# Kernel tuning notes

Measured on AMD Instinct MI355X. Metric: run time of the kernel, lower is better.

Reference implementation:

```python
import jax, jax.numpy as jnp
import numpy as np

HEADS = 8

def setup_inputs() -> dict:
    key = jax.random.key(0)
    ks = jax.random.split(key, 11)
    B, S, E = 4, 2048, 512
    sc = 1.0 / np.sqrt(E)
    return {
        "inputs": jax.random.normal(ks[0], (B, S, E), jnp.float32),
        "entangle": jax.random.uniform(ks[1], (S,), jnp.float32),
        "Wq": jax.random.normal(ks[2], (E, E), jnp.float32) * sc,
        "bq": jax.random.normal(ks[3], (E,), jnp.float32) * 0.01,
        "Wk": jax.random.normal(ks[4], (E, E), jnp.float32) * sc,
        "bk": jax.random.normal(ks[5], (E,), jnp.float32) * 0.01,
        "Wv": jax.random.normal(ks[6], (E, E), jnp.float32) * sc,
        "bv": jax.random.normal(ks[7], (E,), jnp.float32) * 0.01,
        "Wo": jax.random.normal(ks[8], (E, E), jnp.float32) * sc,
        "bo": jax.random.normal(ks[9], (E,), jnp.float32) * 0.01,
    }

def reference(inputs, entangle, Wq, bq, Wk, bk, Wv, bv, Wo, bo):
    B, S, E = inputs.shape
    H = HEADS
    D = E // H
    # torch nn.Linear: y = x @ W.T + b
    Q = (inputs @ Wq.T + bq).reshape(B, S, H, D)
    K = (inputs @ Wk.T + bk).reshape(B, S, H, D)
    V = (inputs @ Wv.T + bv).reshape(B, S, H, D)
    scores = jnp.einsum('bqhd,bkhd->bhqk', Q, K) / jnp.sqrt(jnp.float32(D))
    # entangle broadcast as (1,1,S,1): per-query-position scaling before softmax
    scores = scores * entangle[None, None, :, None]
    attn = jax.nn.softmax(scores, axis=-1)
    out = jnp.einsum('bhqk,bkhd->bqhd', attn, V).reshape(B, S, E)
    return out @ Wo.T + bo
```

## Files before the change

### kernel.cpp

```cpp
#include <hip/hip_runtime.h>
#include <hip/hip_bf16.h>

#define BB 4
#define SS 2048
#define EE 512
#define HH 8
#define DD 64

typedef __attribute__((ext_vector_type(8))) short bf16x8;
typedef __attribute__((ext_vector_type(4))) float f32x4;
typedef __attribute__((ext_vector_type(4))) unsigned int u32x4;

__device__ __forceinline__ unsigned short f2bf(float f) {
    __hip_bfloat16 h = __float2bfloat16(f);
    return *reinterpret_cast<unsigned short*>(&h);
}

__device__ __forceinline__ unsigned int cvtpk(float lo, float hi) {
    unsigned int r;
    asm("v_cvt_pk_bf16_f32 %0, %1, %2" : "=v"(r) : "v"(lo), "v"(hi));
    return r;
}

__device__ __forceinline__ float ex2(float x) {
    float r;
    asm("v_exp_f32 %0, %1" : "=v"(r) : "v"(x));
    return r;
}

__device__ __forceinline__ void pl32(unsigned int& a, unsigned int& b) {
    asm("v_permlane32_swap_b32 %0, %1" : "+v"(a), "+v"(b));
}
__device__ __forceinline__ void pl16(unsigned int& a, unsigned int& b) {
    asm("v_permlane16_swap_b32 %0, %1" : "+v"(a), "+v"(b));
}

__device__ __forceinline__ void gll16(const unsigned short* g, unsigned short* l) {
    __builtin_amdgcn_global_load_lds(
        (const __attribute__((address_space(1))) unsigned int*)g,
        (__attribute__((address_space(3))) unsigned int*)l,
        16, 0, 0);
}

__global__ __launch_bounds__(256)
void cast_all(const float* __restrict__ x,
              const float* __restrict__ wq, const float* __restrict__ wk,
              const float* __restrict__ wv, const float* __restrict__ wo,
              unsigned short* __restrict__ xb,
              unsigned short* __restrict__ wqb, unsigned short* __restrict__ wkb,
              unsigned short* __restrict__ wvb, unsigned short* __restrict__ wob)
{
    const int bid = blockIdx.x;
    const float* src; unsigned short* dst; int lb;
    if (bid < 4096)      { src = x;  dst = xb;  lb = bid; }
    else {
        const int t = (bid - 4096) >> 8;
        lb = (bid - 4096) & 255;
        switch (t) {
            case 0:  src = wq; dst = wqb; break;
            case 1:  src = wk; dst = wkb; break;
            case 2:  src = wv; dst = wvb; break;
            default: src = wo; dst = wob; break;
        }
    }
    const int i = lb * 256 + threadIdx.x;
    const float4 v = reinterpret_cast<const float4*>(src)[i];
    ushort4 o;
    o.x = f2bf(v.x); o.y = f2bf(v.y); o.z = f2bf(v.z); o.w = f2bf(v.w);
    reinterpret_cast<ushort4*>(dst)[i] = o;
}

template<typename OutT, bool TRANSPOSE_V, int TM>
__global__ __launch_bounds__(256)
void gemm_mfma_nt(const unsigned short* __restrict__ A,
                  const unsigned short* __restrict__ W0, const float* __restrict__ b0, OutT* __restrict__ C0,
                  const unsigned short* __restrict__ W1, const float* __restrict__ b1, OutT* __restrict__ C1,
                  const unsigned short* __restrict__ W2, const float* __restrict__ b2, OutT* __restrict__ C2,
                  const float* __restrict__ rowscale,
                  int M, int N, int K)
{
    const unsigned short* W = (blockIdx.z == 0) ? W0 : (blockIdx.z == 1) ? W1 : W2;
    const float* bias       = (blockIdx.z == 0) ? b0 : (blockIdx.z == 1) ? b1 : b2;
    OutT* C                 = (blockIdx.z == 0) ? C0 : (blockIdx.z == 1) ? C1 : C2;

    constexpr int MT  = TM / 32;
    constexpr int STG = 3 * TM * 32;
    __shared__ unsigned short lds[STG + 3 * 128 * 32];
    unsigned short* As = lds;
    unsigned short* Bs = lds + STG;

    const int tid  = threadIdx.x;
    const int wave = tid >> 6, lane = tid & 63;
    const int quad = lane >> 4, r16 = lane & 15;
    const int m0 = blockIdx.x * TM, n0 = blockIdx.y * 128;
    const int wm0 = (wave >> 1) * (TM / 2), wn0 = (wave & 1) * 64;

    f32x4 acc[MT][4];
    const f32x4 zero = {0.f, 0.f, 0.f, 0.f};
    #pragma unroll
    for (int i = 0; i < MT; ++i)
        #pragma unroll
        for (int j = 0; j < 4; ++j) acc[i][j] = zero;

    const int swz = (r16 >> 1) & 3;

    auto stage = [&](int bi, int k0) {
        #pragma unroll
        for (int j = 0; j < TM / 64; ++j) {
            const int cb = wave * 64 + j * 256;
            const int c  = cb + lane;
            const int row = c >> 2, cc = (c & 3) ^ ((row >> 1) & 3);
            gll16(&A[(size_t)(m0 + row) * K + k0 + cc * 8], &As[bi * TM * 32 + cb * 8]);
        }
        #pragma unroll
        for (int j = 0; j < 2; ++j) {
            const int cb = wave * 64 + j * 256;
            const int c  = cb + lane;
            const int row = c >> 2, cc = (c & 3) ^ ((row >> 1) & 3);
            gll16(&W[(size_t)(n0 + row) * K + k0 + cc * 8], &Bs[bi * 128 * 32 + cb * 8]);
        }
    };

    stage(0, 0);
    stage(1, 32);

    const int NI = K / 32;
    for (int i = 0; i < NI; ++i) {
        const int cur = i % 3;
        if (i + 1 < NI) {
            if constexpr (TM == 128) asm volatile("s_waitcnt vmcnt(4)" ::: "memory");
            else                     asm volatile("s_waitcnt vmcnt(3)" ::: "memory");
        } else {
            asm volatile("s_waitcnt vmcnt(0)" ::: "memory");
        }
        __builtin_amdgcn_s_barrier();
        __builtin_amdgcn_sched_barrier(0);
        if (i + 2 < NI) stage((i + 2) % 3, (i + 2) * 32);

        bf16x8 af[MT], bfr[4];
        #pragma unroll
        for (int t = 0; t < MT; ++t)
            af[t]  = *reinterpret_cast<bf16x8*>(&As[cur * TM * 32 + ((wm0 + t * 16 + r16) * 4 + (quad ^ swz)) * 8]);
        #pragma unroll
        for (int t = 0; t < 4; ++t)
            bfr[t] = *reinterpret_cast<bf16x8*>(&Bs[cur * 128 * 32 + ((wn0 + t * 16 + r16) * 4 + (quad ^ swz)) * 8]);
        #pragma unroll
        for (int mt = 0; mt < MT; ++mt)
            #pragma unroll
            for (int nt = 0; nt < 4; ++nt)
                acc[mt][nt] = __builtin_amdgcn_mfma_f32_16x16x32_bf16(
                    af[mt], bfr[nt], acc[mt][nt], 0, 0, 0);
    }

    if (TRANSPOSE_V && blockIdx.z == 2) {
        __syncthreads();
        #pragma unroll
        for (int mt = 0; mt < MT; ++mt) {
            const int s_local = wm0 + mt * 16 + quad * 4;
            #pragma unroll
            for (int nt = 0; nt < 4; ++nt) {
                const int d_local = wn0 + nt * 16 + r16;
                const float bv = bias[n0 + d_local];
                uint2 o;
                o.x = cvtpk(acc[mt][nt][0] + bv, acc[mt][nt][1] + bv);
                o.y = cvtpk(acc[mt][nt][2] + bv, acc[mt][nt][3] + bv);
                *reinterpret_cast<uint2*>(&lds[d_local * 132 + s_local]) = o;
            }
        }
        __syncthreads();
        const int bb = m0 >> 11, s0 = m0 & (SS - 1);
        unsigned short* Vtp = (unsigned short*)C2 + (size_t)bb * EE * SS + s0;
        const int scol = (tid & 15) * 8;
        #pragma unroll
        for (int p = 0; p < 8; ++p) {
            const int row = p * 16 + (tid >> 4);
            const uint2 lo = *reinterpret_cast<const uint2*>(&lds[row * 132 + scol]);
            const uint2 hi = *reinterpret_cast<const uint2*>(&lds[row * 132 + scol + 4]);
            const u32x4 v = {lo.x, lo.y, hi.x, hi.y};
            *reinterpret_cast<u32x4*>(&Vtp[(size_t)(n0 + row) * SS + scol]) = v;
        }
        return;
    }
    if constexpr (sizeof(OutT) == 2) {
        const bool doscale = (rowscale != nullptr) && (blockIdx.z == 0);
        __syncthreads();
        #pragma unroll
        for (int mt = 0; mt < MT; ++mt) {
            float rs[4];
            #pragma unroll
            for (int r = 0; r < 4; ++r) {
                const int row = m0 + wm0 + mt * 16 + quad * 4 + r;
                rs[r] = doscale ? rowscale[row & (SS - 1)] * 0.18033688f : 1.0f;
            }
            #pragma unroll
            for (int nt = 0; nt < 4; ++nt) {
                const int col = wn0 + nt * 16 + r16;
                const float bv = bias[n0 + col];
                #pragma unroll
                for (int r = 0; r < 4; ++r) {
                    const int row = wm0 + mt * 16 + quad * 4 + r;
                    lds[row * 132 + col] = f2bf((acc[mt][nt][r] + bv) * rs[r]);
                }
            }
        }
        __syncthreads();
        const int scol = (tid & 15) * 8;
        #pragma unroll
        for (int p = 0; p < TM / 16; ++p) {
            const int row = p * 16 + (tid >> 4);
            const uint2 lo = *reinterpret_cast<const uint2*>(&lds[row * 132 + scol]);
            const uint2 hi = *reinterpret_cast<const uint2*>(&lds[row * 132 + scol + 4]);
            const u32x4 v = {lo.x, lo.y, hi.x, hi.y};
            *reinterpret_cast<u32x4*>(&((unsigned short*)C)[(size_t)(m0 + row) * N + n0 + scol]) = v;
        }
    } else {
        const bool doscale = (rowscale != nullptr) && (blockIdx.z == 0);
        #pragma unroll
        for (int mt = 0; mt < MT; ++mt) {
            float rs[4];
            #pragma unroll
            for (int r = 0; r < 4; ++r) {
                const int row = m0 + wm0 + mt * 16 + quad * 4 + r;
                rs[r] = doscale ? rowscale[row & (SS - 1)] * 0.18033688f : 1.0f;
            }
            #pragma unroll
            for (int nt = 0; nt < 4; ++nt) {
                const int col = n0 + wn0 + nt * 16 + r16;
                const float bv = bias[col];
                #pragma unroll
                for (int r = 0; r < 4; ++r) {
                    const int row = m0 + wm0 + mt * 16 + quad * 4 + r;
                    C[(size_t)row * N + col] = (OutT)((acc[mt][nt][r] + bv) * rs[r]);
                }
            }
        }
    }
}

#define QBLK 128

__global__ __launch_bounds__(256)
void attn_mfma(const unsigned short* __restrict__ Q,
               const unsigned short* __restrict__ K,
               const unsigned short* __restrict__ Vt,
               unsigned short* __restrict__ O)
{
    __shared__ unsigned short Ks[3][72 * 64];
    __shared__ unsigned short Vs[3][72 * 64];

    const int tid  = threadIdx.x;
    const int wave = tid >> 6, lane = tid & 63;
    const int quad = lane >> 4, r16 = lane & 15;
    const int h  = blockIdx.x;
    const int q0 = blockIdx.y * QBLK;
    const int b  = blockIdx.z;
    const size_t base    = (size_t)b * SS * EE + (size_t)h * DD;
    const size_t base_vt = ((size_t)b * HH + h) * DD * SS;

    bf16x8 qf[2][2];
    #pragma unroll
    for (int s = 0; s < 2; ++s) {
        const int qrow = q0 + s * 64 + wave * 16 + r16;
        #pragma unroll
        for (int dh = 0; dh < 2; ++dh)
            qf[s][dh] = *reinterpret_cast<const bf16x8*>(
                &Q[base + (size_t)qrow * EE + dh * 32 + quad * 8]);
    }

    const int cb0 = wave * 64, cb1 = wave * 64 + 256;
    const int c0 = cb0 + lane, c1 = cb1 + lane;
    const int row0 = c0 >> 3, cc0 = (c0 & 7) ^ (row0 & 7);
    const int row1 = c1 >> 3, cc1 = (c1 & 7) ^ (row1 & 7);
    const unsigned short* kp0 = &K[base + (size_t)row0 * EE + cc0 * 8];
    const unsigned short* kp1 = &K[base + (size_t)row1 * EE + cc1 * 8];
    const unsigned short* vp0 = &Vt[base_vt + (size_t)row0 * SS + cc0 * 8];
    const unsigned short* vp1 = &Vt[base_vt + (size_t)row1 * SS + cc1 * 8];

    auto stage = [&](int bi, int kt) {
        const size_t ko = (size_t)kt * 64 * EE;
        const int    vo = kt * 64;
        gll16(kp0 + ko, &Ks[bi][cb0 * 8]);
        gll16(vp0 + vo, &Vs[bi][cb0 * 8]);
        gll16(kp1 + ko, &Ks[bi][cb1 * 8]);
        gll16(vp1 + vo, &Vs[bi][cb1 * 8]);
    };

    float l_lane[2] = {0.f, 0.f};
    f32x4 o_acc[2][4];
    const f32x4 zero = {0.f, 0.f, 0.f, 0.f};
    #pragma unroll
    for (int s = 0; s < 2; ++s)
        #pragma unroll
        for (int dt = 0; dt < 4; ++dt) o_acc[s][dt] = zero;

    const int swz = r16 & 7;

    stage(0, 0);
    stage(1, 1);

    constexpr int NT = SS / 64;
    for (int kt = 0; kt < NT; ++kt) {
        const int cur = kt % 3;
        if (kt + 1 < NT) asm volatile("s_waitcnt vmcnt(4)" ::: "memory");
        else             asm volatile("s_waitcnt vmcnt(0)" ::: "memory");
        __builtin_amdgcn_s_barrier();
        __builtin_amdgcn_sched_barrier(0);
        if (kt + 2 < NT) stage((kt + 2) % 3, kt + 2);

        const unsigned short* Kc = &Ks[cur][0];
        const unsigned short* Vc = &Vs[cur][0];

        bf16x8 kfA[4], kfB[4];
        #pragma unroll
        for (int tn = 0; tn < 4; ++tn) {
            kfA[tn] = *reinterpret_cast<const bf16x8*>(&Kc[((tn * 16 + r16) * 8 + (quad ^ swz)) * 8]);
            kfB[tn] = *reinterpret_cast<const bf16x8*>(&Kc[((tn * 16 + r16) * 8 + ((quad + 4) ^ swz)) * 8]);
        }

        f32x4 st[2][4];
        #pragma unroll
        for (int s = 0; s < 2; ++s)
            #pragma unroll
            for (int tn = 0; tn < 4; ++tn) st[s][tn] = zero;
        __builtin_amdgcn_s_setprio(1);
        #pragma unroll
        for (int s = 0; s < 2; ++s)
            #pragma unroll
            for (int tn = 0; tn < 4; ++tn) {
                st[s][tn] = __builtin_amdgcn_mfma_f32_16x16x32_bf16(kfA[tn], qf[s][0], st[s][tn], 0, 0, 0);
                st[s][tn] = __builtin_amdgcn_mfma_f32_16x16x32_bf16(kfB[tn], qf[s][1], st[s][tn], 0, 0, 0);
            }
        __builtin_amdgcn_s_setprio(0);

        bf16x8 vfA[4], vfB[4];
        #pragma unroll
        for (int dt = 0; dt < 4; ++dt) {
            vfA[dt] = *reinterpret_cast<const bf16x8*>(&Vc[((dt * 16 + r16) * 8 + (quad ^ swz)) * 8]);
            vfB[dt] = *reinterpret_cast<const bf16x8*>(&Vc[((dt * 16 + r16) * 8 + ((quad + 4) ^ swz)) * 8]);
        }

        #pragma unroll
        for (int s = 0; s < 2; ++s) {
            unsigned int w[4][2];
            #pragma unroll
            for (int tn = 0; tn < 4; ++tn) {
                const float p0 = ex2(st[s][tn][0]);
                const float p1 = ex2(st[s][tn][1]);
                const float p2 = ex2(st[s][tn][2]);
                const float p3 = ex2(st[s][tn][3]);
                l_lane[s] += (p0 + p1) + (p2 + p3);
                w[tn][0] = cvtpk(p0, p1);
                w[tn][1] = cvtpk(p2, p3);
            }
            unsigned int pa0 = w[0][0], pa2 = w[1][0];
            pl32(pa0, pa2); pl16(pa0, pa2);
            unsigned int pa1 = w[0][1], pa3 = w[1][1];
            pl32(pa1, pa3); pl16(pa1, pa3);
            unsigned int pb0 = w[2][0], pb2 = w[3][0];
            pl32(pb0, pb2); pl16(pb0, pb2);
            unsigned int pb1 = w[2][1], pb3 = w[3][1];
            pl32(pb1, pb3); pl16(pb1, pb3);

            const u32x4 ua = {pa0, pa1, pa2, pa3};
            const u32x4 ub = {pb0, pb1, pb2, pb3};
            const bf16x8 pf0 = __builtin_bit_cast(bf16x8, ua);
            const bf16x8 pf1 = __builtin_bit_cast(bf16x8, ub);

            __builtin_amdgcn_s_setprio(1);
            #pragma unroll
            for (int dt = 0; dt < 4; ++dt) {
                o_acc[s][dt] = __builtin_amdgcn_mfma_f32_16x16x32_bf16(pf0, vfA[dt], o_acc[s][dt], 0, 0, 0);
                o_acc[s][dt] = __builtin_amdgcn_mfma_f32_16x16x32_bf16(pf1, vfB[dt], o_acc[s][dt], 0, 0, 0);
            }
            __builtin_amdgcn_s_setprio(0);
        }
    }

    float lq[2];
    #pragma unroll
    for (int s = 0; s < 2; ++s) {
        float l = l_lane[s];
        l += __shfl_xor(l, 16, 64);
        l += __shfl_xor(l, 32, 64);
        lq[s] = l;
    }

    unsigned short* ob = &Ks[0][0];
    __syncthreads();
    #pragma unroll
    for (int s = 0; s < 2; ++s) {
        #pragma unroll
        for (int r = 0; r < 4; ++r) {
            const float il = 1.0f / __shfl(lq[s], quad * 4 + r, 64);
            const int ql = s * 64 + wave * 16 + quad * 4 + r;
            #pragma unroll
            for (int dt = 0; dt < 4; ++dt)
                ob[ql * 68 + dt * 16 + r16] = f2bf(o_acc[s][dt][r] * il);
        }
    }
    __syncthreads();
    const int orow = tid >> 3, ocol = (tid & 7) * 8;
    #pragma unroll
    for (int p = 0; p < 4; ++p) {
        const int ql = p * 32 + orow;
        const uint2 lo = *reinterpret_cast<const uint2*>(&ob[ql * 68 + ocol]);
        const uint2 hi = *reinterpret_cast<const uint2*>(&ob[ql * 68 + ocol + 4]);
        const u32x4 v = {lo.x, lo.y, hi.x, hi.y};
        *reinterpret_cast<u32x4*>(&O[base + (size_t)(q0 + ql) * EE + ocol]) = v;
    }
}

extern "C" void kernel_launch(void* const* d_in, const int* in_sizes, int n_in,
                              void* d_out, int out_size, void* d_ws, size_t ws_size,
                              hipStream_t stream) {
    const float* x   = (const float*)d_in[0];
    const float* ent = (const float*)d_in[1];
    const float* Wq  = (const float*)d_in[2];
    const float* bq  = (const float*)d_in[3];
    const float* Wk  = (const float*)d_in[4];
    const float* bk  = (const float*)d_in[5];
    const float* Wv  = (const float*)d_in[6];
    const float* bv  = (const float*)d_in[7];
    const float* Wo  = (const float*)d_in[8];
    const float* bo  = (const float*)d_in[9];
    float* out = (float*)d_out;

    const size_t n_x = (size_t)BB * SS * EE;
    const size_t n_w = (size_t)EE * EE;

    unsigned short* xb  = (unsigned short*)d_ws;
    unsigned short* wqb = xb + n_x;
    unsigned short* wkb = wqb + n_w;
    unsigned short* wvb = wkb + n_w;
    unsigned short* wob = wvb + n_w;
    unsigned short* Qb  = wob + n_w;
    unsigned short* Kb  = Qb + n_x;
    unsigned short* Vtb = Kb + n_x;
    unsigned short* AOb = Vtb + n_x;

    const int M = BB * SS;

    dim3 gc(4096 + 4 * 256, 1, 1);
    cast_all<<<gc, 256, 0, stream>>>(x, Wq, Wk, Wv, Wo, xb, wqb, wkb, wvb, wob);

    dim3 gq(M / 128, EE / 128, 3);
    gemm_mfma_nt<unsigned short, true, 128><<<gq, 256, 0, stream>>>(
        xb, wqb, bq, Qb, wkb, bk, Kb, wvb, bv, Vtb, ent, M, EE, EE);

    dim3 ga(HH, SS / QBLK, BB);
    attn_mfma<<<ga, 256, 0, stream>>>(Qb, Kb, Vtb, AOb);

    dim3 go(M / 64, EE / 128, 1);
    gemm_mfma_nt<float, false, 64><<<go, 256, 0, stream>>>(
        AOb, wob, bo, out, wob, bo, out, wob, bo, out, nullptr, M, EE, EE);
}
```

Before: 168.8 us.

## Widen attention KV tile to 128 with double buffering and stage fp32 GEMM epilogue via LDS

The attention kernel now processes 128 keys per iteration instead of 64, using two LDS buffers instead of three and a new swizzle for the wider V tile. This halves barrier and waitcnt overhead per key and lets each V fragment load feed both query sub-tiles. The waitcnt becomes vmcnt(0) with only one stage of prefetch, so load latency may be less hidden. Launch bounds add a minimum of two blocks per SM. The GEMM fp32 output path now stages results through LDS and writes coalesced float4 rows, and it drops the rowscale multiplication in that path.

```diff
diff --git a/kernel.cpp b/kernel.cpp
--- a/kernel.cpp
+++ b/kernel.cpp
@@ -214,39 +214,43 @@
             *reinterpret_cast<u32x4*>(&((unsigned short*)C)[(size_t)(m0 + row) * N + n0 + scol]) = v;
         }
     } else {
-        const bool doscale = (rowscale != nullptr) && (blockIdx.z == 0);
+        float* fl = reinterpret_cast<float*>(lds);
+        __syncthreads();
         #pragma unroll
         for (int mt = 0; mt < MT; ++mt) {
-            float rs[4];
-            #pragma unroll
-            for (int r = 0; r < 4; ++r) {
-                const int row = m0 + wm0 + mt * 16 + quad * 4 + r;
-                rs[r] = doscale ? rowscale[row & (SS - 1)] * 0.18033688f : 1.0f;
-            }
             #pragma unroll
             for (int nt = 0; nt < 4; ++nt) {
-                const int col = n0 + wn0 + nt * 16 + r16;
-                const float bv = bias[col];
+                const int col = wn0 + nt * 16 + r16;
+                const float bv = bias[n0 + col];
                 #pragma unroll
                 for (int r = 0; r < 4; ++r) {
-                    const int row = m0 + wm0 + mt * 16 + quad * 4 + r;
-                    C[(size_t)row * N + col] = (OutT)((acc[mt][nt][r] + bv) * rs[r]);
+                    const int row = wm0 + mt * 16 + quad * 4 + r;
+                    fl[row * 132 + col] = acc[mt][nt][r] + bv;
                 }
             }
         }
+        __syncthreads();
+        const int scol = (tid & 31) * 4;
+        #pragma unroll
+        for (int p = 0; p < TM / 8; ++p) {
+            const int row = p * 8 + (tid >> 5);
+            const f32x4 v = *reinterpret_cast<const f32x4*>(&fl[row * 132 + scol]);
+            *reinterpret_cast<f32x4*>(&((float*)C)[(size_t)(m0 + row) * N + n0 + scol]) = v;
+        }
     }
 }
 
 #define QBLK 128
-
-__global__ __launch_bounds__(256)
+#define KVB  128
+
+__global__ __launch_bounds__(256, 2)
 void attn_mfma(const unsigned short* __restrict__ Q,
                const unsigned short* __restrict__ K,
                const unsigned short* __restrict__ Vt,
                unsigned short* __restrict__ O)
 {
-    __shared__ unsigned short Ks[3][72 * 64];
-    __shared__ unsigned short Vs[3][72 * 64];
+    __shared__ unsigned short Ks[2][KVB * 64];
+    __shared__ unsigned short Vs[2][64 * KVB];
 
     const int tid  = threadIdx.x;
     const int wave = tid >> 6, lane = tid & 63;
@@ -267,22 +271,28 @@
                 &Q[base + (size_t)qrow * EE + dh * 32 + quad * 8]);
     }
 
-    const int cb0 = wave * 64, cb1 = wave * 64 + 256;
-    const int c0 = cb0 + lane, c1 = cb1 + lane;
-    const int row0 = c0 >> 3, cc0 = (c0 & 7) ^ (row0 & 7);
-    const int row1 = c1 >> 3, cc1 = (c1 & 7) ^ (row1 & 7);
-    const unsigned short* kp0 = &K[base + (size_t)row0 * EE + cc0 * 8];
-    const unsigned short* kp1 = &K[base + (size_t)row1 * EE + cc1 * 8];
-    const unsigned short* vp0 = &Vt[base_vt + (size_t)row0 * SS + cc0 * 8];
-    const unsigned short* vp1 = &Vt[base_vt + (size_t)row1 * SS + cc1 * 8];
+    const unsigned short* kp[4];
+    const unsigned short* vp[4];
+    int cbs[4];
+    #pragma unroll
+    for (int j = 0; j < 4; ++j) {
+        const int cb = wave * 64 + j * 256;
+        cbs[j] = cb;
+        const int c  = cb + lane;
+        const int rowK = c >> 3, ccK = (c & 7) ^ (rowK & 7);
+        kp[j] = &K[base + (size_t)rowK * EE + ccK * 8];
+        const int rowV = c >> 4, ccV = (c & 15) ^ (rowV & 15);
+        vp[j] = &Vt[base_vt + (size_t)rowV * SS + ccV * 8];
+    }
 
     auto stage = [&](int bi, int kt) {
-        const size_t ko = (size_t)kt * 64 * EE;
-        const int    vo = kt * 64;
-        gll16(kp0 + ko, &Ks[bi][cb0 * 8]);
-        gll16(vp0 + vo, &Vs[bi][cb0 * 8]);
-        gll16(kp1 + ko, &Ks[bi][cb1 * 8]);
-        gll16(vp1 + vo, &Vs[bi][cb1 * 8]);
+        const size_t ko = (size_t)kt * KVB * EE;
+        const int    vo = kt * KVB;
+        #pragma unroll
+        for (int j = 0; j < 4; ++j) {
+            gll16(kp[j] + ko, &Ks[bi][cbs[j] * 8]);
+            gll16(vp[j] + vo, &Vs[bi][cbs[j] * 8]);
+        }
     };
 
     float l_lane[2] = {0.f, 0.f};
@@ -293,57 +303,47 @@
         #pragma unroll
         for (int dt = 0; dt < 4; ++dt) o_acc[s][dt] = zero;
 
-    const int swz = r16 & 7;
+    const int swz7 = r16 & 7;
 
     stage(0, 0);
-    stage(1, 1);
-
-    constexpr int NT = SS / 64;
+
+    constexpr int NT = SS / KVB;
     for (int kt = 0; kt < NT; ++kt) {
-        const int cur = kt % 3;
-        if (kt + 1 < NT) asm volatile("s_waitcnt vmcnt(4)" ::: "memory");
-        else             asm volatile("s_waitcnt vmcnt(0)" ::: "memory");
+        const int cur = kt & 1;
+        asm volatile("s_waitcnt vmcnt(0)" ::: "memory");
         __builtin_amdgcn_s_barrier();
         __builtin_amdgcn_sched_barrier(0);
-        if (kt + 2 < NT) stage((kt + 2) % 3, kt + 2);
+        if (kt + 1 < NT) stage(cur ^ 1, kt + 1);
 
         const unsigned short* Kc = &Ks[cur][0];
         const unsigned short* Vc = &Vs[cur][0];
 
-        bf16x8 kfA[4], kfB[4];
-        #pragma unroll
-        for (int tn = 0; tn < 4; ++tn) {
-            kfA[tn] = *reinterpret_cast<const bf16x8*>(&Kc[((tn * 16 + r16) * 8 + (quad ^ swz)) * 8]);
-            kfB[tn] = *reinterpret_cast<const bf16x8*>(&Kc[((tn * 16 + r16) * 8 + ((quad + 4) ^ swz)) * 8]);
-        }
-
-        f32x4 st[2][4];
+        f32x4 st[2][8];
         #pragma unroll
         for (int s = 0; s < 2; ++s)
             #pragma unroll
-            for (int tn = 0; tn < 4; ++tn) st[s][tn] = zero;
+            for (int tn = 0; tn < 8; ++tn) st[s][tn] = zero;
         __builtin_amdgcn_s_setprio(1);
         #pragma unroll
-        for (int s = 0; s < 2; ++s)
-            #pragma unroll
-            for (int tn = 0; tn < 4; ++tn) {
-                st[s][tn] = __builtin_amdgcn_mfma_f32_16x16x32_bf16(kfA[tn], qf[s][0], st[s][tn], 0, 0, 0);
-                st[s][tn] = __builtin_amdgcn_mfma_f32_16x16x32_bf16(kfB[tn], qf[s][1], st[s][tn], 0, 0, 0);
-            }
+        for (int tn = 0; tn < 8; ++tn) {
+            const bf16x8 kf0 = *reinterpret_cast<const bf16x8*>(
+                &Kc[((tn * 16 + r16) * 8 + (quad ^ swz7)) * 8]);
+            const bf16x8 kf1 = *reinterpret_cast<const bf16x8*>(
+                &Kc[((tn * 16 + r16) * 8 + ((quad + 4) ^ swz7)) * 8]);
+            #pragma unroll
+            for (int s = 0; s < 2; ++s) {
+                st[s][tn] = __builtin_amdgcn_mfma_f32_16x16x32_bf16(kf0, qf[s][0], st[s][tn], 0, 0, 0);
+                st[s][tn] = __builtin_amdgcn_mfma_f32_16x16x32_bf16(kf1, qf[s][1], st[s][tn], 0, 0, 0);
+            }
+        }
         __builtin_amdgcn_s_setprio(0);
 
-        bf16x8 vfA[4], vfB[4];
-        #pragma unroll
-        for (int dt = 0; dt < 4; ++dt) {
-            vfA[dt] = *reinterpret_cast<const bf16x8*>(&Vc[((dt * 16 + r16) * 8 + (quad ^ swz)) * 8]);
-            vfB[dt] = *reinterpret_cast<const bf16x8*>(&Vc[((dt * 16 + r16) * 8 + ((quad + 4) ^ swz)) * 8]);
-        }
-
+        bf16x8 pf[2][4];
         #pragma unroll
         for (int s = 0; s < 2; ++s) {
-            unsigned int w[4][2];
-            #pragma unroll
-            for (int tn = 0; tn < 4; ++tn) {
+            unsigned int w[8][2];
+            #pragma unroll
+            for (int tn = 0; tn < 8; ++tn) {
                 const float p0 = ex2(st[s][tn][0]);
                 const float p1 = ex2(st[s][tn][1]);
                 const float p2 = ex2(st[s][tn][2]);
@@ -352,28 +352,29 @@
                 w[tn][0] = cvtpk(p0, p1);
                 w[tn][1] = cvtpk(p2, p3);
             }
-            unsigned int pa0 = w[0][0], pa2 = w[1][0];
-            pl32(pa0, pa2); pl16(pa0, pa2);
-            unsigned int pa1 = w[0][1], pa3 = w[1][1];
-            pl32(pa1, pa3); pl16(pa1, pa3);
-            unsigned int pb0 = w[2][0], pb2 = w[3][0];
-            pl32(pb0, pb2); pl16(pb0, pb2);
-            unsigned int pb1 = w[2][1], pb3 = w[3][1];
-            pl32(pb1, pb3); pl16(pb1, pb3);
-
-            const u32x4 ua = {pa0, pa1, pa2, pa3};
-            const u32x4 ub = {pb0, pb1, pb2, pb3};
-            const bf16x8 pf0 = __builtin_bit_cast(bf16x8, ua);
-            const bf16x8 pf1 = __builtin_bit_cast(bf16x8, ub);
-
-            __builtin_amdgcn_s_setprio(1);
+            #pragma unroll
+            for (int j = 0; j < 4; ++j) {
+                unsigned int a0 = w[2 * j][0], a2 = w[2 * j + 1][0];
+                pl32(a0, a2); pl16(a0, a2);
+                unsigned int a1 = w[2 * j][1], a3 = w[2 * j + 1][1];
+                pl32(a1, a3); pl16(a1, a3);
+                const u32x4 u = {a0, a1, a2, a3};
+                pf[s][j] = __builtin_bit_cast(bf16x8, u);
+            }
+        }
+
+        __builtin_amdgcn_s_setprio(1);
+        #pragma unroll
+        for (int j = 0; j < 4; ++j) {
             #pragma unroll
             for (int dt = 0; dt < 4; ++dt) {
-                o_acc[s][dt] = __builtin_amdgcn_mfma_f32_16x16x32_bf16(pf0, vfA[dt], o_acc[s][dt], 0, 0, 0);
-                o_acc[s][dt] = __builtin_amdgcn_mfma_f32_16x16x32_bf16(pf1, vfB[dt], o_acc[s][dt], 0, 0, 0);
-            }
-            __builtin_amdgcn_s_setprio(0);
-        }
+                const bf16x8 vf = *reinterpret_cast<const bf16x8*>(
+                    &Vc[((dt * 16 + r16) * 16 + ((4 * j + quad) ^ r16)) * 8]);
+                o_acc[0][dt] = __builtin_amdgcn_mfma_f32_16x16x32_bf16(pf[0][j], vf, o_acc[0][dt], 0, 0, 0);
+                o_acc[1][dt] = __builtin_amdgcn_mfma_f32_16x16x32_bf16(pf[1][j], vf, o_acc[1][dt], 0, 0, 0);
+            }
+        }
+        __builtin_amdgcn_s_setprio(0);
     }
 
     float lq[2];
```

After: 158.2 us. -6.3%, faster.
